# Optimization experiments

Hardware: AMD Instinct MI355X
Metric: run time of the kernel (lower is better)

Reference implementation:

```python
import jax, jax.numpy as jnp
import numpy as np

B, T, I, H = 128, 800, 300, 32  # batch, sl, input dim, hidden


def setup_inputs() -> dict:
    key = jax.random.key(0)
    ks = jax.random.split(key, 10)
    s_h = 1.0 / np.sqrt(H)
    s_t = 1.0 / np.sqrt(T)
    s_f = 1.0 / np.sqrt(H * T)
    u = lambda k, shape, s: jax.random.uniform(k, shape, jnp.float32, -s, s)
    return {
        "x": jax.random.normal(ks[0], (B, T, I), jnp.float32),
        "W_ih": u(ks[1], (4 * H, I), s_h),   # torch gate order: i, f, g, o
        "W_hh": u(ks[2], (4 * H, H), s_h),
        "b_ih": u(ks[3], (4 * H,), s_h),
        "b_hh": u(ks[4], (4 * H,), s_h),
        "Ww": u(ks[5], (T, T), s_t),         # Linear(sl, sl)
        "bw": u(ks[6], (T,), s_t),
        "Wfc": u(ks[7], (1, H * T), s_f),    # Linear(h*sl, 1)
        "bfc": u(ks[8], (1,), s_f),
    }


def _lstm(x, W_ih, W_hh, b_ih, b_hh):
    # Precompute input projections for all timesteps: [B, T, 4H]
    gx = jnp.einsum('bti,gi->btg', x, W_ih) + b_ih + b_hh
    h0 = jnp.zeros((x.shape[0], H), x.dtype)
    c0 = jnp.zeros_like(h0)

    def step(carry, g_t):
        h, c = carry
        g = g_t + h @ W_hh.T  # [B, 4H]
        i_g, f_g, g_g, o_g = jnp.split(g, 4, axis=-1)
        i_g = jax.nn.sigmoid(i_g)
        f_g = jax.nn.sigmoid(f_g)
        g_g = jnp.tanh(g_g)
        o_g = jax.nn.sigmoid(o_g)
        c = f_g * c + i_g * g_g
        h = o_g * jnp.tanh(c)
        return (h, c), h

    _, hs = jax.lax.scan(step, (h0, c0), jnp.swapaxes(gx, 0, 1))  # hs: [T, B, H]
    return jnp.swapaxes(hs, 0, 1)  # [B, T, H]


def reference(x, W_ih, W_hh, b_ih, b_hh, Ww, bw, Wfc, bfc):
    out = _lstm(x, W_ih, W_hh, b_ih, b_hh)  # [B, T, H]
    # permute -> Linear(sl, sl) over the seq axis -> permute back, fused in one einsum
    # q[b, s, h] = sum_t out[b, t, h] * Ww[s, t] + bw[s]
    q = jnp.einsum('bth,st->bsh', out, Ww) + bw[None, :, None]
    qk = out * q  # [B, T, H]
    out_fc = qk.reshape(qk.shape[0], -1) @ Wfc.T + bfc  # [B, 1]
    return (out_fc, qk)
```

## Files before the change

### kernel.cpp

```cpp
#include <hip/hip_runtime.h>
#include <stdint.h>

#define B_SZ 128
#define T_SZ 800
#define I_SZ 300
#define KPAD 320
#define H_SZ 32
#define G_SZ 128
#define NWIN 50
#define NBUF 4
#define TP   808

typedef float f32x4 __attribute__((ext_vector_type(4)));
typedef _Float16 half8 __attribute__((ext_vector_type(8)));
typedef _Float16 half2v __attribute__((ext_vector_type(2)));

union FragH { half8 v; _Float16 h[8]; uint4 u4; };
union PkU  { uint u; _Float16 h[2]; };
union HsU  { ushort s; _Float16 h; };
union Pk2  { uint u; half2v v; };

#if __has_builtin(__builtin_amdgcn_permlane32_swap)
#define HAVE_PL32 1
#else
#define HAVE_PL32 0
#endif

#if __has_builtin(__builtin_amdgcn_fdot2) && __has_builtin(__builtin_amdgcn_mov_dpp)
#define HAVE_DOT2 1
#else
#define HAVE_DOT2 0
#endif

__device__ __forceinline__ float tanhfast(float x) {
    float ax = fabsf(x);
    float z = __expf(-2.f * ax);
    float r = __fdividef(1.f - z, 1.f + z);
    return __builtin_copysignf(r, x);
}
__device__ __forceinline__ float sigmoidf_(float x) {
    return __fdividef(1.f, 1.f + __expf(-x));
}
__device__ __forceinline__ float bcast_lane(float v, int srclane) {
    return __int_as_float(__builtin_amdgcn_readlane(__float_as_int(v), srclane));
}

__global__ __launch_bounds__(256) void k_prep(
    const float* __restrict__ W_ih, const float* __restrict__ Ww,
    _Float16* __restrict__ W_ihH, _Float16* __restrict__ WwH)
{
    int i = blockIdx.x * 256 + threadIdx.x;
    if (i < G_SZ * KPAD) {
        int r = i / KPAD, k = i - r * KPAD;
        W_ihH[i] = (k < I_SZ) ? (_Float16)W_ih[r * I_SZ + k] : (_Float16)0.f;
    }
    int j = i - G_SZ * KPAD;
    if (j >= 0 && j < T_SZ * T_SZ) WwH[j] = (_Float16)Ww[j];
}

__global__ __launch_bounds__(256) void k_main(
    const float* __restrict__ x, const _Float16* __restrict__ W_ihH,
    const float* __restrict__ W_hh,
    const float* __restrict__ b_ih, const float* __restrict__ b_hh,
    const _Float16* __restrict__ WwH, const float* __restrict__ bw,
    const float* __restrict__ Wfc, const float* __restrict__ bfc,
    float* __restrict__ out)
{
    const int b    = blockIdx.x;
    const int tid  = threadIdx.x;
    const int wave = tid >> 6;
    const int lane = tid & 63;
    const int m16  = lane & 15;
    const int quad = lane >> 4;

    __shared__ __align__(16) ushort hist[H_SZ][TP];
    __shared__ __align__(16) uint   gxbuf[NBUF][16][64];
    __shared__ int produced, consumed;
    __shared__ float red[4];

    if (tid == 0) { produced = 0; consumed = 0; }
    __syncthreads();

    if (wave == 0) {
#if HAVE_PL32
        bool pl_pick_x;
        {
            auto t2 = __builtin_amdgcn_permlane32_swap(lane, lane, false, false);
            pl_pick_x = ((int)__builtin_amdgcn_readlane((int)t2[0], 63) < (int)H_SZ);
        }
#endif
        float c = 0.f;

#if HAVE_DOT2 && HAVE_PL32
        uint WpA[16], WpB[16];
#pragma unroll
        for (int j = 0; j < 16; ++j) {
            HsU a0_, a1_, b0_, b1_;
            a0_.h = (_Float16)W_hh[lane * H_SZ + 2*j];
            a1_.h = (_Float16)W_hh[lane * H_SZ + 2*j + 1];
            b0_.h = (_Float16)W_hh[(lane + 64) * H_SZ + 2*j];
            b1_.h = (_Float16)W_hh[(lane + 64) * H_SZ + 2*j + 1];
            WpA[j] = (uint)a0_.s | ((uint)a1_.s << 16);
            WpB[j] = (uint)b0_.s | ((uint)b1_.s << 16);
        }
        int hpk = 0;

        for (int w = 0; w < NWIN; ++w) {
            while (__atomic_load_n(&produced, __ATOMIC_ACQUIRE) < w + 1)
                __builtin_amdgcn_s_sleep(2);
#pragma unroll 4
            for (int tl = 0; tl < 16; ++tl) {
                const int t = w * 16 + tl;
                PkU g; g.u = gxbuf[w & (NBUF - 1)][tl][lane];
                float aA0 = 0.f, aA1 = 0.f, aB0 = 0.f, aB1 = 0.f;
#pragma unroll
                for (int j = 0; j < 16; j += 2) {
                    Pk2 h0; h0.u = (uint)__builtin_amdgcn_readlane(hpk, 32 + 2*j);
                    Pk2 h1; h1.u = (uint)__builtin_amdgcn_readlane(hpk, 32 + 2*j + 2);
                    Pk2 wa0; wa0.u = WpA[j];     Pk2 wb0; wb0.u = WpB[j];
                    Pk2 wa1; wa1.u = WpA[j + 1]; Pk2 wb1; wb1.u = WpB[j + 1];
                    aA0 = __builtin_amdgcn_fdot2(wa0.v, h0.v, aA0, false);
                    aB0 = __builtin_amdgcn_fdot2(wb0.v, h0.v, aB0, false);
                    aA1 = __builtin_amdgcn_fdot2(wa1.v, h1.v, aA1, false);
                    aB1 = __builtin_amdgcn_fdot2(wb1.v, h1.v, aB1, false);
                }
                float g0 = (aA0 + aA1) + (float)g.h[0];
                float g1 = (aB0 + aB1) + (float)g.h[1];

                float a0 = sigmoidf_(g0);
                float zz = (lane < H_SZ) ? g1 : 0.5f * g1;
                float th = tanhfast(zz);
                float a1 = (lane < H_SZ) ? th : 0.5f * th + 0.5f;

                float ig  = a0 * a1;
                auto rr = __builtin_amdgcn_permlane32_swap(
                    __float_as_int(ig), __float_as_int(ig), false, false);
                float igs = __int_as_float(pl_pick_x ? (int)rr[0] : (int)rr[1]);
                c = a0 * c + igs;
                float h = a1 * tanhfast(c);

                HsU hc; hc.h = (_Float16)h;
                uint hcu = (uint)hc.s;
                uint hnb = (uint)__builtin_amdgcn_mov_dpp((int)hcu, 0xB1, 0xF, 0xF, false);
                hpk = (int)((hnb << 16) | hcu);
                if (lane >= H_SZ)
                    hist[lane - H_SZ][t] = hc.s;
            }
            __atomic_store_n(&consumed, w + 1, __ATOMIC_RELEASE);
        }
#else
        float W0[H_SZ], W1[H_SZ];
#pragma unroll
        for (int k = 0; k < H_SZ; ++k) W0[k] = W_hh[lane * H_SZ + k];
#pragma unroll
        for (int k = 0; k < H_SZ; ++k) W1[k] = W_hh[(lane + 64) * H_SZ + k];
        float hprev = 0.f;

        for (int w = 0; w < NWIN; ++w) {
            while (__atomic_load_n(&produced, __ATOMIC_ACQUIRE) < w + 1)
                __builtin_amdgcn_s_sleep(2);
#pragma unroll 4
            for (int tl = 0; tl < 16; ++tl) {
                const int t = w * 16 + tl;
                PkU g; g.u = gxbuf[w & (NBUF - 1)][tl][lane];
                float p0=0.f,p1=0.f,p2=0.f,p3=0.f;
                float q0=0.f,q1=0.f,q2=0.f,q3=0.f;
#pragma unroll
                for (int k = 0; k < H_SZ; k += 4) {
                    float h0 = bcast_lane(hprev, H_SZ + k + 0);
                    float h1 = bcast_lane(hprev, H_SZ + k + 1);
                    float h2 = bcast_lane(hprev, H_SZ + k + 2);
                    float h3 = bcast_lane(hprev, H_SZ + k + 3);
                    p0 += W0[k+0]*h0; q0 += W1[k+0]*h0;
                    p1 += W0[k+1]*h1; q1 += W1[k+1]*h1;
                    p2 += W0[k+2]*h2; q2 += W1[k+2]*h2;
                    p3 += W0[k+3]*h3; q3 += W1[k+3]*h3;
                }
                float g0 = ((p0 + p1) + (p2 + p3)) + (float)g.h[0];
                float g1 = ((q0 + q1) + (q2 + q3)) + (float)g.h[1];

                float a0 = sigmoidf_(g0);
                float zz = (lane < H_SZ) ? g1 : 0.5f * g1;
                float th = tanhfast(zz);
                float a1 = (lane < H_SZ) ? th : 0.5f * th + 0.5f;

                float ig  = a0 * a1;
                float igs = __shfl_up(ig, 32, 64);
                c = a0 * c + igs;
                float h = a1 * tanhfast(c);
                hprev = h;
                if (lane >= H_SZ) {
                    HsU hs; hs.h = (_Float16)h;
                    hist[lane - H_SZ][t] = hs.s;
                }
            }
            __atomic_store_n(&consumed, w + 1, __ATOMIC_RELEASE);
        }
#endif
    } else {
        float bias[8];
#pragma unroll
        for (int nt = 0; nt < 8; ++nt)
            bias[nt] = b_ih[nt * 16 + m16] + b_hh[nt * 16 + m16];
        const float* xb = x + (size_t)b * T_SZ * I_SZ;

        for (int w = wave - 1; w < NWIN; w += 3) {
            const float* xrow = xb + (size_t)(w * 16 + m16) * I_SZ;
            f32x4 acc[8];
#pragma unroll
            for (int nt = 0; nt < 8; ++nt) acc[nt] = (f32x4){0.f, 0.f, 0.f, 0.f};

            for (int ks = 0; ks < 9; ++ks) {
                const int k0 = ks * 32 + quad * 8;
                f32x4 x0 = *(const f32x4*)(xrow + k0);
                f32x4 x1 = *(const f32x4*)(xrow + k0 + 4);
                FragH a;
                a.h[0] = (_Float16)x0[0]; a.h[1] = (_Float16)x0[1];
                a.h[2] = (_Float16)x0[2]; a.h[3] = (_Float16)x0[3];
                a.h[4] = (_Float16)x1[0]; a.h[5] = (_Float16)x1[1];
                a.h[6] = (_Float16)x1[2]; a.h[7] = (_Float16)x1[3];
#pragma unroll
                for (int nt = 0; nt < 8; ++nt) {
                    FragH bb;
                    bb.u4 = *(const uint4*)(W_ihH + (size_t)(nt * 16 + m16) * KPAD + k0);
                    acc[nt] = __builtin_amdgcn_mfma_f32_16x16x32_f16(a.v, bb.v, acc[nt], 0, 0, 0);
                }
            }
            {
                FragH a;
#pragma unroll
                for (int jj = 0; jj < 8; ++jj) {
                    int k = 288 + quad * 8 + jj;
                    a.h[jj] = (k < I_SZ) ? (_Float16)xrow[k] : (_Float16)0.f;
                }
#pragma unroll
                for (int nt = 0; nt < 8; ++nt) {
                    FragH bb;
                    bb.u4 = *(const uint4*)(W_ihH + (size_t)(nt * 16 + m16) * KPAD + 288 + quad * 8);
                    acc[nt] = __builtin_amdgcn_mfma_f32_16x16x32_f16(a.v, bb.v, acc[nt], 0, 0, 0);
                }
            }
            while (__atomic_load_n(&consumed, __ATOMIC_ACQUIRE) < w - (NBUF - 1))
                __builtin_amdgcn_s_sleep(8);
#pragma unroll
            for (int nt = 0; nt < 4; ++nt)
#pragma unroll
                for (int r = 0; r < 4; ++r) {
                    PkU p;
                    p.h[0] = (_Float16)(acc[nt][r]     + bias[nt]);
                    p.h[1] = (_Float16)(acc[nt + 4][r] + bias[nt + 4]);
                    gxbuf[w & (NBUF - 1)][quad * 4 + r][nt * 16 + m16] = p.u;
                }
            while (__atomic_load_n(&produced, __ATOMIC_ACQUIRE) != w)
                __builtin_amdgcn_s_sleep(8);
            __atomic_store_n(&produced, w + 1, __ATOMIC_RELEASE);
        }
    }
    __syncthreads();

    float* region = out + B_SZ + (size_t)b * T_SZ * H_SZ;
    float fc_acc = 0.f;

    for (int st = wave; st < T_SZ / 16; st += 4) {
        const int s0 = st * 16;
        f32x4 acc0 = (f32x4){0.f,0.f,0.f,0.f};
        f32x4 acc1 = (f32x4){0.f,0.f,0.f,0.f};
        const _Float16* wwrow = WwH + (size_t)(s0 + m16) * T_SZ;

        for (int t0 = 0; t0 < T_SZ; t0 += 32) {
            FragH a, b0, b1;
            a.u4  = *(const uint4*)(wwrow + t0 + quad * 8);
            b0.u4 = *(const uint4*)&hist[m16][t0 + quad * 8];
            b1.u4 = *(const uint4*)&hist[16 + m16][t0 + quad * 8];
            acc0 = __builtin_amdgcn_mfma_f32_16x16x32_f16(a.v, b0.v, acc0, 0, 0, 0);
            acc1 = __builtin_amdgcn_mfma_f32_16x16x32_f16(a.v, b1.v, acc1, 0, 0, 0);
        }
#pragma unroll
        for (int r = 0; r < 4; ++r) {
            int s = s0 + quad * 4 + r;
            float bws = bw[s];
            HsU u0; u0.s = hist[m16][s];      float h0 = (float)u0.h;
            HsU u1; u1.s = hist[16 + m16][s]; float h1 = (float)u1.h;
            float q0 = acc0[r] + bws;
            float q1 = acc1[r] + bws;
            float qk0 = h0 * q0;
            float qk1 = h1 * q1;
            region[(size_t)s * H_SZ + m16]      = qk0;
            region[(size_t)s * H_SZ + 16 + m16] = qk1;
            fc_acc += qk0 * Wfc[s * H_SZ + m16];
            fc_acc += qk1 * Wfc[s * H_SZ + 16 + m16];
        }
    }

#pragma unroll
    for (int off = 32; off > 0; off >>= 1)
        fc_acc += __shfl_down(fc_acc, off, 64);
    if (lane == 0) red[wave] = fc_acc;
    __syncthreads();
    if (tid == 0) out[b] = red[0] + red[1] + red[2] + red[3] + bfc[0];
}

extern "C" void kernel_launch(void* const* d_in, const int* in_sizes, int n_in,
                              void* d_out, int out_size, void* d_ws, size_t ws_size,
                              hipStream_t stream) {
    const float* x    = (const float*)d_in[0];
    const float* W_ih = (const float*)d_in[1];
    const float* W_hh = (const float*)d_in[2];
    const float* b_ih = (const float*)d_in[3];
    const float* b_hh = (const float*)d_in[4];
    const float* Ww   = (const float*)d_in[5];
    const float* bw   = (const float*)d_in[6];
    const float* Wfc  = (const float*)d_in[7];
    const float* bfc  = (const float*)d_in[8];

    float* out = (float*)d_out;

    _Float16* W_ihH = (_Float16*)d_ws;
    _Float16* WwH   = (_Float16*)((char*)d_ws + (size_t)G_SZ * KPAD * 2);

    int prep_n = G_SZ * KPAD + T_SZ * T_SZ;
    k_prep<<<(prep_n + 255) / 256, 256, 0, stream>>>(W_ih, Ww, W_ihH, WwH);
    k_main<<<B_SZ, 256, 0, stream>>>(x, W_ihH, W_hh, b_ih, b_hh, WwH, bw, Wfc, bfc, out);
}
```

Baseline: 408.1 us.

## Split attention epilogue into separate kernel parallelized over batch and tile groups

The LSTM kernel now writes the fp16 hidden-state history to a global workspace instead of shared memory. The Ww projection, qk and fc reduction move into a new kernel launched on a (batch, 13 group) grid, with the fc sum combined through atomicAdd. Previously that stage ran on only 128 blocks after the serial recurrence. The split spreads it over many more CUs, at the cost of an extra launch, a global round trip for the history, and float atomics whose summation order is not deterministic.

Result: no change. 414.2 us (+1.5%).

```diff
diff --git a/kernel.cpp b/kernel.cpp
--- a/kernel.cpp
+++ b/kernel.cpp
@@ -10,6 +10,8 @@
 #define NWIN 50
 #define NBUF 4
 #define TP   808
+#define NTILE 50
+#define NGRP 13
 
 typedef float f32x4 __attribute__((ext_vector_type(4)));
 typedef _Float16 half8 __attribute__((ext_vector_type(8)));
@@ -62,8 +64,8 @@
     const float* __restrict__ x, const _Float16* __restrict__ W_ihH,
     const float* __restrict__ W_hh,
     const float* __restrict__ b_ih, const float* __restrict__ b_hh,
-    const _Float16* __restrict__ WwH, const float* __restrict__ bw,
-    const float* __restrict__ Wfc, const float* __restrict__ bfc,
+    const float* __restrict__ bfc,
+    _Float16* __restrict__ histG,
     float* __restrict__ out)
 {
     const int b    = blockIdx.x;
@@ -73,12 +75,10 @@
     const int m16  = lane & 15;
     const int quad = lane >> 4;
 
-    __shared__ __align__(16) ushort hist[H_SZ][TP];
-    __shared__ __align__(16) uint   gxbuf[NBUF][16][64];
+    __shared__ __align__(16) uint gxbuf[NBUF][16][64];
     __shared__ int produced, consumed;
-    __shared__ float red[4];
-
-    if (tid == 0) { produced = 0; consumed = 0; }
+
+    if (tid == 0) { produced = 0; consumed = 0; out[b] = bfc[0]; }
     __syncthreads();
 
     if (wave == 0) {
@@ -90,6 +90,7 @@
         }
 #endif
         float c = 0.f;
+        _Float16* hG = histG + (size_t)b * H_SZ * T_SZ + (size_t)(lane - H_SZ) * T_SZ;
 
 #if HAVE_DOT2 && HAVE_PL32
         uint WpA[16], WpB[16];
@@ -144,7 +145,7 @@
                 uint hnb = (uint)__builtin_amdgcn_mov_dpp((int)hcu, 0xB1, 0xF, 0xF, false);
                 hpk = (int)((hnb << 16) | hcu);
                 if (lane >= H_SZ)
-                    hist[lane - H_SZ][t] = hc.s;
+                    hG[t] = hc.h;
             }
             __atomic_store_n(&consumed, w + 1, __ATOMIC_RELEASE);
         }
@@ -189,10 +190,7 @@
                 c = a0 * c + igs;
                 float h = a1 * tanhfast(c);
                 hprev = h;
-                if (lane >= H_SZ) {
-                    HsU hs; hs.h = (_Float16)h;
-                    hist[lane - H_SZ][t] = hs.s;
-                }
+                if (lane >= H_SZ) hG[t] = (_Float16)h;
             }
             __atomic_store_n(&consumed, w + 1, __ATOMIC_RELEASE);
         }
@@ -256,48 +254,70 @@
             __atomic_store_n(&produced, w + 1, __ATOMIC_RELEASE);
         }
     }
+}
+
+__global__ __launch_bounds__(256) void k_attn(
+    const _Float16* __restrict__ histG, const _Float16* __restrict__ WwH,
+    const float* __restrict__ bw, const float* __restrict__ Wfc,
+    float* __restrict__ out)
+{
+    const int b    = blockIdx.x;
+    const int grp  = blockIdx.y;
+    const int tid  = threadIdx.x;
+    const int wave = tid >> 6;
+    const int lane = tid & 63;
+    const int m16  = lane & 15;
+    const int quad = lane >> 4;
+
+    __shared__ __align__(16) ushort histL[H_SZ][TP];
+
+    const _Float16* hb = histG + (size_t)b * H_SZ * T_SZ;
+    for (int i = tid; i < H_SZ * (T_SZ / 8); i += 256) {
+        int r = i / (T_SZ / 8), c = i - r * (T_SZ / 8);
+        *(uint4*)&histL[r][c * 8] = *(const uint4*)(hb + (size_t)r * T_SZ + c * 8);
+    }
     __syncthreads();
 
+    const int st = grp * 4 + wave;
+    if (st >= NTILE) return;
+    const int s0 = st * 16;
+
     float* region = out + B_SZ + (size_t)b * T_SZ * H_SZ;
+    f32x4 acc0 = (f32x4){0.f,0.f,0.f,0.f};
+    f32x4 acc1 = (f32x4){0.f,0.f,0.f,0.f};
+    const _Float16* wwrow = WwH + (size_t)(s0 + m16) * T_SZ;
+
+#pragma unroll 2
+    for (int t0 = 0; t0 < T_SZ; t0 += 32) {
+        FragH a, b0, b1;
+        a.u4  = *(const uint4*)(wwrow + t0 + quad * 8);
+        b0.u4 = *(const uint4*)&histL[m16][t0 + quad * 8];
+        b1.u4 = *(const uint4*)&histL[16 + m16][t0 + quad * 8];
+        acc0 = __builtin_amdgcn_mfma_f32_16x16x32_f16(a.v, b0.v, acc0, 0, 0, 0);
+        acc1 = __builtin_amdgcn_mfma_f32_16x16x32_f16(a.v, b1.v, acc1, 0, 0, 0);
+    }
+
     float fc_acc = 0.f;
-
-    for (int st = wave; st < T_SZ / 16; st += 4) {
-        const int s0 = st * 16;
-        f32x4 acc0 = (f32x4){0.f,0.f,0.f,0.f};
-        f32x4 acc1 = (f32x4){0.f,0.f,0.f,0.f};
-        const _Float16* wwrow = WwH + (size_t)(s0 + m16) * T_SZ;
-
-        for (int t0 = 0; t0 < T_SZ; t0 += 32) {
-            FragH a, b0, b1;
-            a.u4  = *(const uint4*)(wwrow + t0 + quad * 8);
-            b0.u4 = *(const uint4*)&hist[m16][t0 + quad * 8];
-            b1.u4 = *(const uint4*)&hist[16 + m16][t0 + quad * 8];
-            acc0 = __builtin_amdgcn_mfma_f32_16x16x32_f16(a.v, b0.v, acc0, 0, 0, 0);
-            acc1 = __builtin_amdgcn_mfma_f32_16x16x32_f16(a.v, b1.v, acc1, 0, 0, 0);
-        }
-#pragma unroll
-        for (int r = 0; r < 4; ++r) {
-            int s = s0 + quad * 4 + r;
-            float bws = bw[s];
-            HsU u0; u0.s = hist[m16][s];      float h0 = (float)u0.h;
-            HsU u1; u1.s = hist[16 + m16][s]; float h1 = (float)u1.h;
-            float q0 = acc0[r] + bws;
-            float q1 = acc1[r] + bws;
-            float qk0 = h0 * q0;
-            float qk1 = h1 * q1;
-            region[(size_t)s * H_SZ + m16]      = qk0;
-            region[(size_t)s * H_SZ + 16 + m16] = qk1;
-            fc_acc += qk0 * Wfc[s * H_SZ + m16];
-            fc_acc += qk1 * Wfc[s * H_SZ + 16 + m16];
-        }
+#pragma unroll
+    for (int r = 0; r < 4; ++r) {
+        int s = s0 + quad * 4 + r;
+        float bws = bw[s];
+        HsU u0; u0.s = histL[m16][s];      float h0 = (float)u0.h;
+        HsU u1; u1.s = histL[16 + m16][s]; float h1 = (float)u1.h;
+        float q0 = acc0[r] + bws;
+        float q1 = acc1[r] + bws;
+        float qk0 = h0 * q0;
+        float qk1 = h1 * q1;
+        region[(size_t)s * H_SZ + m16]      = qk0;
+        region[(size_t)s * H_SZ + 16 + m16] = qk1;
+        fc_acc += qk0 * Wfc[s * H_SZ + m16];
+        fc_acc += qk1 * Wfc[s * H_SZ + 16 + m16];
     }
 
 #pragma unroll
     for (int off = 32; off > 0; off >>= 1)
         fc_acc += __shfl_down(fc_acc, off, 64);
-    if (lane == 0) red[wave] = fc_acc;
-    __syncthreads();
-    if (tid == 0) out[b] = red[0] + red[1] + red[2] + red[3] + bfc[0];
+    if (lane == 0) atomicAdd(out + b, fc_acc);
 }
 
 extern "C" void kernel_launch(void* const* d_in, const int* in_sizes, int n_in,
@@ -317,8 +337,11 @@
 
     _Float16* W_ihH = (_Float16*)d_ws;
     _Float16* WwH   = (_Float16*)((char*)d_ws + (size_t)G_SZ * KPAD * 2);
+    _Float16* histG = (_Float16*)((char*)d_ws + (size_t)G_SZ * KPAD * 2
+                                             + (size_t)T_SZ * T_SZ * 2);
 
     int prep_n = G_SZ * KPAD + T_SZ * T_SZ;
     k_prep<<<(prep_n + 255) / 256, 256, 0, stream>>>(W_ih, Ww, W_ihH, WwH);
-    k_main<<<B_SZ, 256, 0, stream>>>(x, W_ihH, W_hh, b_ih, b_hh, WwH, bw, Wfc, bfc, out);
-}
+    k_main<<<B_SZ, 256, 0, stream>>>(x, W_ihH, W_hh, b_ih, b_hh, bfc, histG, out);
+    k_attn<<<dim3(B_SZ, NGRP), 256, 0, stream>>>(histG, WwH, bw, Wfc, out);
+}
```
